# Performance work log

Hardware: AMD Instinct MI355X
Metric: run time of the kernel (lower is better)

Reference implementation:

```python
import jax, jax.numpy as jnp
import numpy as np

N_NODES = 100000
N_EDGES = 600000
D = 128
HEADS = 8
REL = 9
N_GRAPHS = 64


def _relconv(h, coeff, basis, w_loop, b, src, dst, etypes, n_nodes):
    # DGL RelGraphConv, basis regularizer (num_bases == num_rels), sum aggregation,
    # self-loop, bias, relu activation (dropout inactive at eval).
    W = jnp.einsum('rb,bio->rio', coeff, basis)  # [REL, D, D]
    hsrc = h[src]                                # [E, D] gather
    msg = jnp.zeros((hsrc.shape[0], W.shape[2]), h.dtype)
    for r in range(REL):  # small fixed relation set
        msg = msg + jnp.where((etypes == r)[:, None], hsrc @ W[r], 0.0)
    agg = jax.ops.segment_sum(msg, dst, num_segments=n_nodes)
    return jax.nn.relu(agg + h @ w_loop + b)


def _graph_norm(x, seg, n_graphs, w, b, ms):
    # scatter-based per-subgraph normalization (graphNorm)
    counts = jax.ops.segment_sum(jnp.ones((x.shape[0],), x.dtype), seg, num_segments=n_graphs)[:, None]
    mean = jax.ops.segment_sum(x, seg, num_segments=n_graphs) / counts
    sub = x - mean[seg] * ms
    var = jax.ops.segment_sum(sub * sub, seg, num_segments=n_graphs) / counts
    std = jnp.sqrt(var + 1e-6)
    return w * sub / std[seg] + b


def _layer_norm(x, g, b):
    mu = x.mean(-1, keepdims=True)
    v = jnp.mean((x - mu) ** 2, -1, keepdims=True)
    return g * (x - mu) / jnp.sqrt(v + 1e-5) + b


def _forward(h, src, dst, etypes, seg, num_graphs,
             q_coeff, q_basis, q_loop, q_bias,
             k_coeff, k_basis, k_loop, k_bias,
             v_coeff, v_basis, v_loop, v_bias,
             o_w, o_b, gn1_w, gn1_b, gn1_ms, ln1_g, ln1_b,
             gn2_w, gn2_b, gn2_ms, ffn1_w, ffn1_b, ffn2_w, ffn2_b,
             ln2_g, ln2_b):
    n = h.shape[0]
    hn = _graph_norm(h, seg, num_graphs, gn1_w, gn1_b, gn1_ms)
    Q = _relconv(hn, q_coeff, q_basis, q_loop, q_bias, src, dst, etypes, n)
    K = _relconv(hn, k_coeff, k_basis, k_loop, k_bias, src, dst, etypes, n)
    V = _relconv(hn, v_coeff, v_basis, v_loop, v_bias, src, dst, etypes, n)
    dh = D // HEADS
    Qh = Q.reshape(n, HEADS, dh)
    Kh = K.reshape(n, HEADS, dh)
    Vh = V.reshape(n, HEADS, dh)
    # edge dot-product attention: score_e = <K[src], Q[dst]> per head
    score = (Kh[src] * Qh[dst]).sum(-1, keepdims=True)            # [E, H, 1]
    score = jnp.exp(jnp.clip(score / np.float32(np.sqrt(dh)), -10.0, 10.0))
    wV = jax.ops.segment_sum(Vh[src] * score, dst, num_segments=n)  # [N, H, dh]
    z = jax.ops.segment_sum(score, dst, num_segments=n)             # [N, H, 1]
    attn = (wV / (z + 1e-6)).reshape(n, D)
    hO = attn @ o_w + o_b
    h1 = _layer_norm(hO, ln1_g, ln1_b)
    h2 = _graph_norm(h1, seg, num_graphs, gn2_w, gn2_b, gn2_ms)
    h3 = jax.nn.relu(h2 @ ffn1_w + ffn1_b) @ ffn2_w + ffn2_b
    return _layer_norm(h3, ln2_g, ln2_b)


def setup_inputs() -> dict:
    key = jax.random.key(0)
    ks = jax.random.split(key, 32)
    s = np.float32(1.0 / np.sqrt(D))
    inp = {
        'h': jax.random.normal(ks[0], (N_NODES, D), jnp.float32),
        'src': jax.random.randint(ks[1], (N_EDGES,), 0, N_NODES),
        'dst': jax.random.randint(ks[2], (N_EDGES,), 0, N_NODES),
        'etypes': jax.random.randint(ks[3], (N_EDGES,), 0, REL),
        'seg': jnp.sort(jax.random.randint(ks[4], (N_NODES,), 0, N_GRAPHS)),
        'num_graphs': N_GRAPHS,
    }
    def lin(k, i, o):
        return jax.random.normal(k, (i, o), jnp.float32) / np.float32(np.sqrt(i))
    for idx, nm in enumerate(['q', 'k', 'v']):
        base = 5 + idx * 4
        inp[nm + '_coeff'] = jax.random.normal(ks[base], (REL, REL), jnp.float32) / np.float32(np.sqrt(REL))
        inp[nm + '_basis'] = jax.random.normal(ks[base + 1], (REL, D, D), jnp.float32) * s
        inp[nm + '_loop'] = lin(ks[base + 2], D, D)
        inp[nm + '_bias'] = jnp.zeros((D,), jnp.float32)
    inp['o_w'] = lin(ks[17], D, D)
    inp['o_b'] = jnp.zeros((D,), jnp.float32)
    for nm in ['gn1', 'gn2']:
        inp[nm + '_w'] = jnp.ones((D,), jnp.float32)
        inp[nm + '_b'] = jnp.zeros((D,), jnp.float32)
        inp[nm + '_ms'] = jnp.ones((D,), jnp.float32)
    inp['ln1_g'] = jnp.ones((D,), jnp.float32)
    inp['ln1_b'] = jnp.zeros((D,), jnp.float32)
    inp['ln2_g'] = jnp.ones((D,), jnp.float32)
    inp['ln2_b'] = jnp.zeros((D,), jnp.float32)
    inp['ffn1_w'] = lin(ks[18], D, 2 * D)
    inp['ffn1_b'] = jnp.zeros((2 * D,), jnp.float32)
    inp['ffn2_w'] = lin(ks[19], 2 * D, D)
    inp['ffn2_b'] = jnp.zeros((D,), jnp.float32)
    return inp


def reference(h, src, dst, etypes, seg, num_graphs,
              q_coeff, q_basis, q_loop, q_bias,
              k_coeff, k_basis, k_loop, k_bias,
              v_coeff, v_basis, v_loop, v_bias,
              o_w, o_b, gn1_w, gn1_b, gn1_ms, ln1_g, ln1_b,
              gn2_w, gn2_b, gn2_ms, ffn1_w, ffn1_b, ffn2_w, ffn2_b,
              ln2_g, ln2_b):
    return _forward(h, src, dst, etypes, seg, num_graphs,
                    q_coeff, q_basis, q_loop, q_bias,
                    k_coeff, k_basis, k_loop, k_bias,
                    v_coeff, v_basis, v_loop, v_bias,
                    o_w, o_b, gn1_w, gn1_b, gn1_ms, ln1_g, ln1_b,
                    gn2_w, gn2_b, gn2_ms, ffn1_w, ffn1_b, ffn2_w, ffn2_b,
                    ln2_g, ln2_b)
```

## Files before the change

kernel.cpp:

```cpp
#include <hip/hip_runtime.h>
#include <math.h>

#define N_NODES 100000
#define N_EDGES 600000
#define D 128
#define REL 9
#define NG 64

typedef float f32x4 __attribute__((ext_vector_type(4)));
typedef _Float16 f16x8 __attribute__((ext_vector_type(8)));
typedef _Float16 h16x2 __attribute__((ext_vector_type(2)));

__device__ __forceinline__ ushort f2h(float x) {
    union { _Float16 h; ushort u; } c; c.h = (_Float16)x; return c.u;
}
__device__ __forceinline__ float h2f(ushort u) {
    union { ushort u; _Float16 h; } c; c.u = u; return (float)c.h;
}

__device__ __forceinline__ void ld16(const ushort* g, ushort* l) {
    __builtin_amdgcn_global_load_lds(
        (const __attribute__((address_space(1))) unsigned int*)g,
        (__attribute__((address_space(3))) unsigned int*)l, 16, 0, 0);
}

__device__ __forceinline__ int lbound(const int* __restrict__ a, int n, int key) {
    int lo = 0, hi = n;
    while (lo < hi) { int mid = (lo + hi) >> 1; if (a[mid] < key) lo = mid + 1; else hi = mid; }
    return lo;
}

__global__ void hist_kernel(const int* __restrict__ dst, int* __restrict__ cnt) {
    int e = blockIdx.x * 256 + threadIdx.x;
    if (e < N_EDGES) atomicAdd(&cnt[dst[e]], 1);
}

__global__ void scan1_kernel(const int* __restrict__ cnt, int* __restrict__ excl,
                             int* __restrict__ bsum, int n) {
    __shared__ int s[1024];
    int tid = threadIdx.x;
    int i = blockIdx.x * 1024 + tid;
    int v = (i < n) ? cnt[i] : 0;
    s[tid] = v;
    __syncthreads();
    for (int off = 1; off < 1024; off <<= 1) {
        int t = (tid >= off) ? s[tid - off] : 0;
        __syncthreads();
        s[tid] += t;
        __syncthreads();
    }
    if (i < n) excl[i] = s[tid] - v;
    if (tid == 1023) bsum[blockIdx.x] = s[1023];
}

__global__ void scan2_kernel(int* __restrict__ bsum, int nb) {
    __shared__ int s[128];
    int tid = threadIdx.x;
    int v = (tid < nb) ? bsum[tid] : 0;
    s[tid] = v;
    __syncthreads();
    for (int off = 1; off < 128; off <<= 1) {
        int t = (tid >= off) ? s[tid - off] : 0;
        __syncthreads();
        s[tid] += t;
        __syncthreads();
    }
    if (tid < nb) bsum[tid] = s[tid] - v;
}

__global__ void scan3_kernel(int* __restrict__ excl, const int* __restrict__ bsum, int n) {
    int i = blockIdx.x * 1024 + threadIdx.x;
    if (i < n) excl[i] += bsum[blockIdx.x];
}

__global__ void scatter_kernel(const int* __restrict__ src, const int* __restrict__ dst,
                               const int* __restrict__ ety, const int* __restrict__ estart,
                               int* __restrict__ cur, int* __restrict__ ssrc,
                               int* __restrict__ setp) {
    int e = blockIdx.x * 256 + threadIdx.x;
    if (e < N_EDGES) {
        int d = dst[e];
        int pos = estart[d] + atomicAdd(&cur[d], 1);
        ssrc[pos] = src[e];
        setp[pos] = ety[e];
    }
}

__global__ __launch_bounds__(256)
void gn_stats(const float* __restrict__ x, const int* __restrict__ seg,
              float* __restrict__ gsum, float* __restrict__ gsumsq) {
    int ch = threadIdx.x & 127;
    int rr = threadIdx.x >> 7;
    int n0 = blockIdx.x * 128;
    int nend = min(n0 + 128, N_NODES);
    float sx = 0.f, sxx = 0.f;
    int cg = -1;
    for (int n = n0 + rr; n < nend; n += 2) {
        int g = seg[n];
        if (g != cg) {
            if (cg >= 0) { atomicAdd(&gsum[cg * D + ch], sx); atomicAdd(&gsumsq[cg * D + ch], sxx); }
            cg = g; sx = 0.f; sxx = 0.f;
        }
        float v = x[(size_t)n * D + ch];
        sx += v; sxx += v * v;
    }
    if (cg >= 0) { atomicAdd(&gsum[cg * D + ch], sx); atomicAdd(&gsumsq[cg * D + ch], sxx); }
}

__global__ __launch_bounds__(256)
void gn_stats_h(const ushort* __restrict__ x, const int* __restrict__ seg,
                float* __restrict__ gsum, float* __restrict__ gsumsq) {
    int ch = threadIdx.x & 127;
    int rr = threadIdx.x >> 7;
    int n0 = blockIdx.x * 128;
    int nend = min(n0 + 128, N_NODES);
    float sx = 0.f, sxx = 0.f;
    int cg = -1;
    for (int n = n0 + rr; n < nend; n += 2) {
        int g = seg[n];
        if (g != cg) {
            if (cg >= 0) { atomicAdd(&gsum[cg * D + ch], sx); atomicAdd(&gsumsq[cg * D + ch], sxx); }
            cg = g; sx = 0.f; sxx = 0.f;
        }
        float v = h2f(x[(size_t)n * D + ch]);
        sx += v; sxx += v * v;
    }
    if (cg >= 0) { atomicAdd(&gsum[cg * D + ch], sx); atomicAdd(&gsumsq[cg * D + ch], sxx); }
}

__global__ void gn_final(const float* __restrict__ gsum, const float* __restrict__ gsumsq,
                         const int* __restrict__ seg, const float* __restrict__ w,
                         const float* __restrict__ b, const float* __restrict__ ms,
                         float* __restrict__ sc, float* __restrict__ off) {
    int g = blockIdx.x, ch = threadIdx.x;
    int lo = lbound(seg, N_NODES, g), hi = lbound(seg, N_NODES, g + 1);
    float cnt = (float)max(hi - lo, 1);
    float mean = gsum[g * D + ch] / cnt;
    float mm = mean * ms[ch];
    float var = gsumsq[g * D + ch] / cnt - 2.f * mm * mean + mm * mm;
    float rstd = rsqrtf(var + 1e-6f);
    float s = w[ch] * rstd;
    sc[g * D + ch] = s;
    off[g * D + ch] = b[ch] - s * mm;
}

__global__ __launch_bounds__(256)
void gn_apply(const float* __restrict__ x, const int* __restrict__ seg,
              const float* __restrict__ sc, const float* __restrict__ off,
              ushort* __restrict__ outhf) {
    int t = blockIdx.x * 256 + threadIdx.x;
    int n = t >> 6;
    if (n >= N_NODES) return;
    int ch = (t & 63) * 2;
    int g = seg[n];
    float2 xv = *(const float2*)&x[(size_t)n * D + ch];
    float2 s2 = *(const float2*)&sc[g * D + ch];
    float2 o2 = *(const float2*)&off[g * D + ch];
    ushort2 o;
    o.x = f2h(s2.x * xv.x + o2.x);
    o.y = f2h(s2.y * xv.y + o2.y);
    *(ushort2*)&outhf[(size_t)n * D + ch] = o;
}

__global__ __launch_bounds__(256)
void gn_apply_h(const ushort* __restrict__ x, const int* __restrict__ seg,
                const float* __restrict__ sc, const float* __restrict__ off,
                ushort* __restrict__ outhf) {
    int t = blockIdx.x * 256 + threadIdx.x;
    int n = t >> 6;
    if (n >= N_NODES) return;
    int ch = (t & 63) * 2;
    int g = seg[n];
    ushort2 xv = *(const ushort2*)&x[(size_t)n * D + ch];
    float2 s2 = *(const float2*)&sc[g * D + ch];
    float2 o2 = *(const float2*)&off[g * D + ch];
    ushort2 o;
    o.x = f2h(s2.x * h2f(xv.x) + o2.x);
    o.y = f2h(s2.y * h2f(xv.y) + o2.y);
    *(ushort2*)&outhf[(size_t)n * D + ch] = o;
}

__global__ void build_bt_qkv3(const float* __restrict__ c0, const float* __restrict__ c1,
                              const float* __restrict__ c2, const float* __restrict__ b0,
                              const float* __restrict__ b1, const float* __restrict__ b2,
                              const float* __restrict__ l0, const float* __restrict__ l1,
                              const float* __restrict__ l2, const float* __restrict__ i0,
                              const float* __restrict__ i1, const float* __restrict__ i2,
                              ushort* __restrict__ Btqkv, float* __restrict__ biasq) {
    int pj = blockIdx.y;
    const float* coeff  = pj == 0 ? c0 : (pj == 1 ? c1 : c2);
    const float* basis  = pj == 0 ? b0 : (pj == 1 ? b1 : b2);
    const float* loop_w = pj == 0 ? l0 : (pj == 1 ? l1 : l2);
    const float* bin    = pj == 0 ? i0 : (pj == 1 ? i1 : i2);
    ushort* Bt = Btqkv + (size_t)pj * 128 * 1280;
    int t = blockIdx.x * 256 + threadIdx.x;
    if (t < 128) biasq[pj * 128 + t] = bin[t];
    if (t >= 128 * 1280) return;
    int o = t / 1280;
    int k = t - o * 1280;
    float v;
    if (k < 128) {
        v = loop_w[k * 128 + o];
    } else {
        int kk = k - 128;
        int r = kk >> 7, i = kk & 127;
        v = 0.f;
#pragma unroll
        for (int b = 0; b < REL; ++b)
            v += coeff[r * REL + b] * basis[((size_t)b * 128 + i) * 128 + o];
    }
    Bt[(size_t)o * 1280 + k] = f2h(v);
}

__global__ void transpose_cast3(const float* __restrict__ o_w, ushort* __restrict__ Bto,
                                const float* __restrict__ f1, ushort* __restrict__ Btf1,
                                const float* __restrict__ f2, ushort* __restrict__ Btf2) {
    int t = blockIdx.x * 256 + threadIdx.x;
    if (t < 16384) {
        int n = t >> 7, k = t & 127;
        Bto[(size_t)n * 128 + k] = f2h(o_w[(size_t)k * 128 + n]);
    } else if (t < 49152) {
        int u = t - 16384;
        int n = u >> 7, k = u & 127;
        Btf1[(size_t)n * 128 + k] = f2h(f1[(size_t)k * 256 + n]);
    } else if (t < 81920) {
        int u = t - 49152;
        int n = u >> 8, k = u & 255;
        Btf2[(size_t)n * 256 + k] = f2h(f2[(size_t)k * 128 + n]);
    }
}

__global__ __launch_bounds__(256)
void s_pass(const ushort* __restrict__ hnhf, const int* __restrict__ ssrc,
            const int* __restrict__ setp, const int* __restrict__ estart,
            const int* __restrict__ ecnt, ushort* __restrict__ Ab, int c0, int c1) {
    int n = c0 + ((blockIdx.x * 256 + threadIdx.x) >> 6);
    if (n >= c1) return;
    int lane = threadIdx.x & 63;
    int e0 = estart[n], e1 = e0 + ecnt[n];
    h16x2 a0 = (h16x2)0, a1 = (h16x2)0, a2 = (h16x2)0, a3 = (h16x2)0, a4 = (h16x2)0;
    h16x2 a5 = (h16x2)0, a6 = (h16x2)0, a7 = (h16x2)0, a8 = (h16x2)0;
#define ACC(rr, hv) switch (rr) { \
        case 0: a0 += hv; break; case 1: a1 += hv; break; case 2: a2 += hv; break; \
        case 3: a3 += hv; break; case 4: a4 += hv; break; case 5: a5 += hv; break; \
        case 6: a6 += hv; break; case 7: a7 += hv; break; default: a8 += hv; break; }
    int e = e0;
    for (; e + 2 <= e1; e += 2) {
        int s0 = ssrc[e], s1 = ssrc[e + 1];
        int r0 = __builtin_amdgcn_readfirstlane(setp[e]);
        int r1 = __builtin_amdgcn_readfirstlane(setp[e + 1]);
        h16x2 hv0 = *(const h16x2*)&hnhf[(size_t)s0 * D + 2 * lane];
        h16x2 hv1 = *(const h16x2*)&hnhf[(size_t)s1 * D + 2 * lane];
        ACC(r0, hv0)
        ACC(r1, hv1)
    }
    if (e < e1) {
        int s0 = ssrc[e];
        int r0 = __builtin_amdgcn_readfirstlane(setp[e]);
        h16x2 hv0 = *(const h16x2*)&hnhf[(size_t)s0 * D + 2 * lane];
        ACC(r0, hv0)
    }
#undef ACC
    ushort* arow = Ab + (size_t)(n - c0) * 1152;
#define ST(r) *(h16x2*)&arow[r * 128 + 2 * lane] = a##r;
    ST(0) ST(1) ST(2) ST(3) ST(4) ST(5) ST(6) ST(7) ST(8)
#undef ST
}

template<bool SPLITA, bool RELU, bool F16OUT>
__global__ __launch_bounds__(256, 3)
void mfma_gemm(const ushort* __restrict__ A1, const ushort* __restrict__ A2, int lda2, int M,
               const ushort* __restrict__ Bt, int K,
               const float* __restrict__ bias, void* __restrict__ Cout, int ldc) {
    __shared__ ushort As[128 * 64];
    __shared__ ushort Bs[128 * 64];
    const int tid = threadIdx.x;
    const int lane = tid & 63;
    const int wave = tid >> 6;
    const int wm = wave & 1, wn = wave >> 1;
    const int quad = lane >> 4, l16 = lane & 15;
    const int col0 = blockIdx.x * 128, row0 = blockIdx.y * 128;

    const ushort* sA1[4];
    const ushort* sA2[4];
    const ushort* sB[4];
#pragma unroll
    for (int i = 0; i < 4; ++i) {
        int rs = (wave * 4 + i) * 8 + (lane >> 3);
        int kg = (lane & 7) ^ (rs & 7);
        int ra = row0 + rs; if (ra >= M) ra = M - 1;
        sA1[i] = SPLITA ? (A1 + (size_t)ra * 128 + kg * 8) : nullptr;
        sA2[i] = A2 + (size_t)ra * lda2 + kg * 8;
        sB[i]  = Bt + (size_t)(col0 + rs) * K + kg * 8;
    }

    f32x4 acc[4][4];
#pragma unroll
    for (int i = 0; i < 4; ++i)
#pragma unroll
        for (int j = 0; j < 4; ++j) acc[i][j] = (f32x4){0.f, 0.f, 0.f, 0.f};

    for (int kc = 0; kc < K; kc += 64) {
#pragma unroll
        for (int i = 0; i < 4; ++i) {
            const ushort* as = (SPLITA && kc < 128) ? (sA1[i] + kc) : (sA2[i] + (SPLITA ? kc - 128 : kc));
            ld16(as, &As[(wave * 4 + i) * 512]);
            ld16(sB[i] + kc, &Bs[(wave * 4 + i) * 512]);
        }
        __syncthreads();
#pragma unroll
        for (int h = 0; h < 2; ++h) {
            f16x8 af[4], bf[4];
#pragma unroll
            for (int i = 0; i < 4; ++i) {
                int r = wm * 64 + i * 16 + l16;
                af[i] = *(const f16x8*)&As[r * 64 + (((h * 4 + quad) ^ (r & 7)) * 8)];
                int c = wn * 64 + i * 16 + l16;
                bf[i] = *(const f16x8*)&Bs[c * 64 + (((h * 4 + quad) ^ (c & 7)) * 8)];
            }
#pragma unroll
            for (int i = 0; i < 4; ++i)
#pragma unroll
                for (int j = 0; j < 4; ++j)
                    acc[i][j] = __builtin_amdgcn_mfma_f32_16x16x32_f16(af[i], bf[j], acc[i][j], 0, 0, 0);
        }
        __syncthreads();
    }

#pragma unroll
    for (int i = 0; i < 4; ++i) {
        int gr0 = row0 + wm * 64 + i * 16 + quad * 4;
#pragma unroll
        for (int r = 0; r < 4; ++r) {
            int grow = gr0 + r;
            if (grow >= M) continue;
#pragma unroll
            for (int j = 0; j < 4; ++j) {
                int gcol = col0 + wn * 64 + j * 16 + l16;
                float v = acc[i][j][r] + bias[gcol];
                if (RELU) v = fmaxf(v, 0.f);
                if (F16OUT) ((ushort*)Cout)[(size_t)grow * ldc + gcol] = f2h(v);
                else        ((float*)Cout)[(size_t)grow * ldc + gcol] = v;
            }
        }
    }
}

template<bool F16OUT>
__global__ __launch_bounds__(256, 3)
void mfma_gemm_ln(const ushort* __restrict__ A, int lda, int M,
                  const ushort* __restrict__ Bt, int K,
                  const float* __restrict__ bias, const float* __restrict__ lng,
                  const float* __restrict__ lnb, void* __restrict__ Cout) {
    __shared__ ushort As[128 * 64];
    __shared__ ushort Bs[128 * 64];
    __shared__ float rsum[2][128];
    __shared__ float rsq[2][128];
    const int tid = threadIdx.x;
    const int lane = tid & 63;
    const int wave = tid >> 6;
    const int wm = wave & 1, wn = wave >> 1;
    const int quad = lane >> 4, l16 = lane & 15;
    const int row0 = blockIdx.y * 128;

    const ushort* sA[4];
    const ushort* sB[4];
#pragma unroll
    for (int i = 0; i < 4; ++i) {
        int rs = (wave * 4 + i) * 8 + (lane >> 3);
        int kg = (lane & 7) ^ (rs & 7);
        int ra = row0 + rs; if (ra >= M) ra = M - 1;
        sA[i] = A + (size_t)ra * lda + kg * 8;
        sB[i] = Bt + (size_t)rs * K + kg * 8;
    }

    f32x4 acc[4][4];
#pragma unroll
    for (int i = 0; i < 4; ++i)
#pragma unroll
        for (int j = 0; j < 4; ++j) acc[i][j] = (f32x4){0.f, 0.f, 0.f, 0.f};

    for (int kc = 0; kc < K; kc += 64) {
#pragma unroll
        for (int i = 0; i < 4; ++i) {
            ld16(sA[i] + kc, &As[(wave * 4 + i) * 512]);
            ld16(sB[i] + kc, &Bs[(wave * 4 + i) * 512]);
        }
        __syncthreads();
#pragma unroll
        for (int h = 0; h < 2; ++h) {
            f16x8 af[4], bf[4];
#pragma unroll
            for (int i = 0; i < 4; ++i) {
                int r = wm * 64 + i * 16 + l16;
                af[i] = *(const f16x8*)&As[r * 64 + (((h * 4 + quad) ^ (r & 7)) * 8)];
                int c = wn * 64 + i * 16 + l16;
                bf[i] = *(const f16x8*)&Bs[c * 64 + (((h * 4 + quad) ^ (c & 7)) * 8)];
            }
#pragma unroll
            for (int i = 0; i < 4; ++i)
#pragma unroll
                for (int j = 0; j < 4; ++j)
                    acc[i][j] = __builtin_amdgcn_mfma_f32_16x16x32_f16(af[i], bf[j], acc[i][j], 0, 0, 0);
        }
        __syncthreads();
    }

#pragma unroll
    for (int i = 0; i < 4; ++i) {
#pragma unroll
        for (int r = 0; r < 4; ++r) {
            float s = 0.f, q = 0.f;
#pragma unroll
            for (int j = 0; j < 4; ++j) {
                float v = acc[i][j][r] + bias[wn * 64 + j * 16 + l16];
                s += v; q += v * v;
            }
            s += __shfl_xor(s, 1); q += __shfl_xor(q, 1);
            s += __shfl_xor(s, 2); q += __shfl_xor(q, 2);
            s += __shfl_xor(s, 4); q += __shfl_xor(q, 4);
            s += __shfl_xor(s, 8); q += __shfl_xor(q, 8);
            if (l16 == 0) {
                int row = wm * 64 + i * 16 + quad * 4 + r;
                rsum[wn][row] = s;
                rsq[wn][row] = q;
            }
        }
    }
    __syncthreads();

#pragma unroll
    for (int i = 0; i < 4; ++i) {
#pragma unroll
        for (int r = 0; r < 4; ++r) {
            int row = wm * 64 + i * 16 + quad * 4 + r;
            int grow = row0 + row;
            if (grow >= M) continue;
            float tot = rsum[0][row] + rsum[1][row];
            float tq  = rsq[0][row] + rsq[1][row];
            float mu = tot * (1.f / 128.f);
            float var = tq * (1.f / 128.f) - mu * mu;
            float rstd = rsqrtf(var + 1e-5f);
#pragma unroll
            for (int j = 0; j < 4; ++j) {
                int gcol = wn * 64 + j * 16 + l16;
                float v = acc[i][j][r] + bias[gcol];
                float o = lng[gcol] * (v - mu) * rstd + lnb[gcol];
                if (F16OUT) ((ushort*)Cout)[(size_t)grow * 128 + gcol] = f2h(o);
                else        ((float*)Cout)[(size_t)grow * 128 + gcol] = o;
            }
        }
    }
}

__global__ __launch_bounds__(256)
void attn_kernel(const ushort* __restrict__ C, const int* __restrict__ ssrc,
                 const int* __restrict__ estart, const int* __restrict__ ecnt,
                 ushort* __restrict__ attnhf) {
    int n = (blockIdx.x * 256 + threadIdx.x) >> 6;
    if (n >= N_NODES) return;
    int lane = threadIdx.x & 63;
    h16x2 qh = *(const h16x2*)&C[(size_t)n * 384 + 2 * lane];
    int e0 = estart[n], e1 = e0 + ecnt[n];
    float wvx = 0.f, wvy = 0.f, z = 0.f;
    int e = e0;
    for (; e + 2 <= e1; e += 2) {
        int s0 = ssrc[e], s1 = ssrc[e + 1];
        h16x2 k0 = *(const h16x2*)&C[(size_t)s0 * 384 + 128 + 2 * lane];
        h16x2 k1 = *(const h16x2*)&C[(size_t)s1 * 384 + 128 + 2 * lane];
        h16x2 v0 = *(const h16x2*)&C[(size_t)s0 * 384 + 256 + 2 * lane];
        h16x2 v1 = *(const h16x2*)&C[(size_t)s1 * 384 + 256 + 2 * lane];
        float d0 = __builtin_amdgcn_fdot2(k0, qh, 0.f, false);
        float d1 = __builtin_amdgcn_fdot2(k1, qh, 0.f, false);
        d0 += __shfl_xor(d0, 1); d1 += __shfl_xor(d1, 1);
        d0 += __shfl_xor(d0, 2); d1 += __shfl_xor(d1, 2);
        d0 += __shfl_xor(d0, 4); d1 += __shfl_xor(d1, 4);
        float sc0 = __expf(fminf(fmaxf(d0 * 0.25f, -10.f), 10.f));
        float sc1 = __expf(fminf(fmaxf(d1 * 0.25f, -10.f), 10.f));
        wvx += sc0 * (float)v0.x + sc1 * (float)v1.x;
        wvy += sc0 * (float)v0.y + sc1 * (float)v1.y;
        z += sc0 + sc1;
    }
    if (e < e1) {
        int s0 = ssrc[e];
        h16x2 k0 = *(const h16x2*)&C[(size_t)s0 * 384 + 128 + 2 * lane];
        h16x2 v0 = *(const h16x2*)&C[(size_t)s0 * 384 + 256 + 2 * lane];
        float d0 = __builtin_amdgcn_fdot2(k0, qh, 0.f, false);
        d0 += __shfl_xor(d0, 1);
        d0 += __shfl_xor(d0, 2);
        d0 += __shfl_xor(d0, 4);
        float sc0 = __expf(fminf(fmaxf(d0 * 0.25f, -10.f), 10.f));
        wvx += sc0 * (float)v0.x;
        wvy += sc0 * (float)v0.y;
        z += sc0;
    }
    float inv = 1.f / (z + 1e-6f);
    ushort2 o;
    o.x = f2h(wvx * inv);
    o.y = f2h(wvy * inv);
    *(ushort2*)&attnhf[(size_t)n * D + 2 * lane] = o;
}

extern "C" void kernel_launch(void* const* d_in, const int* in_sizes, int n_in,
                              void* d_out, int out_size, void* d_ws, size_t ws_size,
                              hipStream_t stream) {
    (void)in_sizes; (void)n_in; (void)out_size;
    const float* h     = (const float*)d_in[0];
    const int*   src   = (const int*)d_in[1];
    const int*   dst   = (const int*)d_in[2];
    const int*   ety   = (const int*)d_in[3];
    const int*   seg   = (const int*)d_in[4];
    const float* coeffs[3] = {(const float*)d_in[6],  (const float*)d_in[10], (const float*)d_in[14]};
    const float* bases [3] = {(const float*)d_in[7],  (const float*)d_in[11], (const float*)d_in[15]};
    const float* loops [3] = {(const float*)d_in[8],  (const float*)d_in[12], (const float*)d_in[16]};
    const float* pbias [3] = {(const float*)d_in[9],  (const float*)d_in[13], (const float*)d_in[17]};
    const float* o_w   = (const float*)d_in[18];
    const float* o_b   = (const float*)d_in[19];
    const float* gn1_w = (const float*)d_in[20];
    const float* gn1_b = (const float*)d_in[21];
    const float* gn1_ms= (const float*)d_in[22];
    const float* gn2_w = (const float*)d_in[23];
    const float* gn2_b = (const float*)d_in[24];
    const float* gn2_ms= (const float*)d_in[25];
    const float* ln1_g = (const float*)d_in[26];
    const float* ln1_b = (const float*)d_in[27];
    const float* ln2_g = (const float*)d_in[28];
    const float* ln2_b = (const float*)d_in[29];
    const float* ffn1_w= (const float*)d_in[30];
    const float* ffn1_b= (const float*)d_in[31];
    const float* ffn2_w= (const float*)d_in[32];
    const float* ffn2_b= (const float*)d_in[33];

    char* p = (char*)d_ws;
    auto take = [&](size_t bytes) { char* r = p; p += (bytes + 255) & ~(size_t)255; return r; };
    int*    ecnt   = (int*)take((size_t)N_NODES * 4);
    int*    ecur   = (int*)take((size_t)N_NODES * 4);
    int*    estart = (int*)take((size_t)N_NODES * 4);
    int*    bsum   = (int*)take(512);
    int*    ssrc   = (int*)take((size_t)N_EDGES * 4);
    int*    setp   = (int*)take((size_t)N_EDGES * 4);
    float*  gsum   = (float*)take((size_t)NG * D * 4 * 2);
    float*  gsumsq = gsum + NG * D;
    float*  gsc    = (float*)take((size_t)NG * D * 4);
    float*  goff   = (float*)take((size_t)NG * D * 4);
    ushort* Btqkv  = (ushort*)take((size_t)384 * 1280 * 2);
    float*  biasq  = (float*)take(384 * 4);
    ushort* Bto    = (ushort*)take((size_t)128 * 128 * 2);
    ushort* Btf1   = (ushort*)take((size_t)256 * 128 * 2);
    ushort* Btf2   = (ushort*)take((size_t)128 * 256 * 2);
    ushort* hnhf   = (ushort*)take((size_t)N_NODES * D * 2);
    ushort* attnhf = (ushort*)take((size_t)N_NODES * D * 2);
    ushort* h1hf   = (ushort*)take((size_t)N_NODES * D * 2);
    ushort* Cqkv   = (ushort*)take((size_t)N_NODES * 384 * 2);
    size_t used = (size_t)(p - (char*)d_ws);
    size_t avail = (ws_size > used) ? ws_size - used : 0;
    int NC = 1;
    if (avail < (size_t)N_NODES * 1152 * 2) NC = 4;
    if (NC == 4 && avail < ((size_t)(N_NODES / 4 + 1) * 1152 * 2)) NC = 8;
    ushort* Ab = (ushort*)p;
    const int chunk = (N_NODES + NC - 1) / NC;

    ushort* gn2hf  = Cqkv;
    ushort* ffn1hf = (ushort*)((char*)Cqkv + 25600000);

    const int EB = (N_EDGES + 255) / 256;
    const int SB = (N_NODES + 1023) / 1024;
    const int WB = (N_NODES * 64 + 255) / 256;
    const int GB = (N_NODES + 127) / 128;
    const int RB = (N_NODES + 127) / 128;

    hipMemsetAsync(ecnt, 0, (size_t)((char*)(estart) - (char*)ecnt), stream);
    hist_kernel<<<EB, 256, 0, stream>>>(dst, ecnt);
    scan1_kernel<<<SB, 1024, 0, stream>>>(ecnt, estart, bsum, N_NODES);
    scan2_kernel<<<1, 128, 0, stream>>>(bsum, SB);
    scan3_kernel<<<SB, 1024, 0, stream>>>(estart, bsum, N_NODES);
    scatter_kernel<<<EB, 256, 0, stream>>>(src, dst, ety, estart, ecur, ssrc, setp);

    build_bt_qkv3<<<dim3(640, 3), 256, 0, stream>>>(
        coeffs[0], coeffs[1], coeffs[2], bases[0], bases[1], bases[2],
        loops[0], loops[1], loops[2], pbias[0], pbias[1], pbias[2], Btqkv, biasq);
    transpose_cast3<<<320, 256, 0, stream>>>(o_w, Bto, ffn1_w, Btf1, ffn2_w, Btf2);

    hipMemsetAsync(gsum, 0, (size_t)NG * D * 8, stream);
    gn_stats<<<GB, 256, 0, stream>>>(h, seg, gsum, gsumsq);
    gn_final<<<NG, 128, 0, stream>>>(gsum, gsumsq, seg, gn1_w, gn1_b, gn1_ms, gsc, goff);
    gn_apply<<<WB, 256, 0, stream>>>(h, seg, gsc, goff, hnhf);

    for (int c = 0; c < NC; ++c) {
        int c0 = c * chunk;
        int c1 = min(N_NODES, c0 + chunk);
        int rows = c1 - c0;
        if (rows <= 0) break;
        s_pass<<<(rows + 3) / 4, 256, 0, stream>>>(hnhf, ssrc, setp, estart, ecnt, Ab, c0, c1);
        mfma_gemm<true, true, true><<<dim3(3, (rows + 127) / 128), 256, 0, stream>>>(
            hnhf + (size_t)c0 * 128, Ab, 1152, rows, Btqkv, 1280, biasq,
            Cqkv + (size_t)c0 * 384, 384);
    }

    attn_kernel<<<WB, 256, 0, stream>>>(Cqkv, ssrc, estart, ecnt, attnhf);

    mfma_gemm_ln<true><<<dim3(1, RB), 256, 0, stream>>>(
        attnhf, 128, N_NODES, Bto, 128, o_b, ln1_g, ln1_b, h1hf);

    hipMemsetAsync(gsum, 0, (size_t)NG * D * 8, stream);
    gn_stats_h<<<GB, 256, 0, stream>>>(h1hf, seg, gsum, gsumsq);
    gn_final<<<NG, 128, 0, stream>>>(gsum, gsumsq, seg, gn2_w, gn2_b, gn2_ms, gsc, goff);
    gn_apply_h<<<WB, 256, 0, stream>>>(h1hf, seg, gsc, goff, gn2hf);

    mfma_gemm<false, true, true><<<dim3(2, RB), 256, 0, stream>>>(
        nullptr, gn2hf, 128, N_NODES, Btf1, 128, ffn1_b, ffn1hf, 256);
    mfma_gemm_ln<false><<<dim3(1, RB), 256, 0, stream>>>(
        ffn1hf, 256, N_NODES, Btf2, 256, ffn2_b, ln2_g, ln2_b, (float*)d_out);
}
```

Before: 769.8 us.

## Fuse per-relation neighbor aggregation into the QKV GEMM via relation-sorted CSR

Edges are now bucketed by (destination, relation) with a 9x-larger histogram and scan, so each node's edges of each relation are contiguous. The separate s_pass kernel that wrote a 1152-wide aggregated A matrix to global memory is removed. Instead a new 512-thread QKV GEMM gathers and sums neighbor features for each relation K-chunk directly into shared memory and covers all 384 output columns in one block. This drops the large intermediate write and read, but puts irregular gathers inside the GEMM's K loop without pipelining, and the gathers are repeated for both 64-wide halves of each relation.

```diff
diff --git a/kernel.cpp b/kernel.cpp
--- a/kernel.cpp
+++ b/kernel.cpp
@@ -6,6 +6,7 @@
 #define D 128
 #define REL 9
 #define NG 64
+#define NK9 (N_NODES * REL)
 
 typedef float f32x4 __attribute__((ext_vector_type(4)));
 typedef _Float16 f16x8 __attribute__((ext_vector_type(8)));
@@ -30,18 +31,21 @@
     return lo;
 }
 
-__global__ void hist_kernel(const int* __restrict__ dst, int* __restrict__ cnt) {
+__global__ void hist9_kernel(const int* __restrict__ dst, const int* __restrict__ ety,
+                             int* __restrict__ cnt9) {
     int e = blockIdx.x * 256 + threadIdx.x;
-    if (e < N_EDGES) atomicAdd(&cnt[dst[e]], 1);
-}
-
-__global__ void scan1_kernel(const int* __restrict__ cnt, int* __restrict__ excl,
-                             int* __restrict__ bsum, int n) {
+    if (e < N_EDGES) atomicAdd(&cnt9[dst[e] * REL + ety[e]], 1);
+}
+
+__global__ void scan1_8(const int* __restrict__ cnt, int* __restrict__ excl,
+                        int* __restrict__ bsum, int n) {
     __shared__ int s[1024];
     int tid = threadIdx.x;
-    int i = blockIdx.x * 1024 + tid;
-    int v = (i < n) ? cnt[i] : 0;
-    s[tid] = v;
+    int base = blockIdx.x * 8192 + tid * 8;
+    int v[8]; int sum = 0;
+#pragma unroll
+    for (int j = 0; j < 8; ++j) { v[j] = (base + j < n) ? cnt[base + j] : 0; sum += v[j]; }
+    s[tid] = sum;
     __syncthreads();
     for (int off = 1; off < 1024; off <<= 1) {
         int t = (tid >= off) ? s[tid - off] : 0;
@@ -49,7 +53,9 @@
         s[tid] += t;
         __syncthreads();
     }
-    if (i < n) excl[i] = s[tid] - v;
+    int run = s[tid] - sum;
+#pragma unroll
+    for (int j = 0; j < 8; ++j) { if (base + j < n) excl[base + j] = run; run += v[j]; }
     if (tid == 1023) bsum[blockIdx.x] = s[1023];
 }
 
@@ -68,21 +74,22 @@
     if (tid < nb) bsum[tid] = s[tid] - v;
 }
 
-__global__ void scan3_kernel(int* __restrict__ excl, const int* __restrict__ bsum, int n) {
-    int i = blockIdx.x * 1024 + threadIdx.x;
-    if (i < n) excl[i] += bsum[blockIdx.x];
-}
-
-__global__ void scatter_kernel(const int* __restrict__ src, const int* __restrict__ dst,
-                               const int* __restrict__ ety, const int* __restrict__ estart,
-                               int* __restrict__ cur, int* __restrict__ ssrc,
-                               int* __restrict__ setp) {
+__global__ void scan3_8(int* __restrict__ excl, const int* __restrict__ bsum, int n, int total) {
+    int base = blockIdx.x * 8192 + threadIdx.x * 8;
+    int add = bsum[blockIdx.x];
+#pragma unroll
+    for (int j = 0; j < 8; ++j) if (base + j < n) excl[base + j] += add;
+    if (blockIdx.x == 0 && threadIdx.x == 0) excl[n] = total;
+}
+
+__global__ void scatter9_kernel(const int* __restrict__ src, const int* __restrict__ dst,
+                                const int* __restrict__ ety, const int* __restrict__ rstart,
+                                int* __restrict__ cur9, int* __restrict__ ssrc) {
     int e = blockIdx.x * 256 + threadIdx.x;
     if (e < N_EDGES) {
-        int d = dst[e];
-        int pos = estart[d] + atomicAdd(&cur[d], 1);
+        int key = dst[e] * REL + ety[e];
+        int pos = rstart[key] + atomicAdd(&cur9[key], 1);
         ssrc[pos] = src[e];
-        setp[pos] = ety[e];
     }
 }
 
@@ -230,41 +237,111 @@
     }
 }
 
-__global__ __launch_bounds__(256)
-void s_pass(const ushort* __restrict__ hnhf, const int* __restrict__ ssrc,
-            const int* __restrict__ setp, const int* __restrict__ estart,
-            const int* __restrict__ ecnt, ushort* __restrict__ Ab, int c0, int c1) {
-    int n = c0 + ((blockIdx.x * 256 + threadIdx.x) >> 6);
-    if (n >= c1) return;
-    int lane = threadIdx.x & 63;
-    int e0 = estart[n], e1 = e0 + ecnt[n];
-    h16x2 a0 = (h16x2)0, a1 = (h16x2)0, a2 = (h16x2)0, a3 = (h16x2)0, a4 = (h16x2)0;
-    h16x2 a5 = (h16x2)0, a6 = (h16x2)0, a7 = (h16x2)0, a8 = (h16x2)0;
-#define ACC(rr, hv) switch (rr) { \
-        case 0: a0 += hv; break; case 1: a1 += hv; break; case 2: a2 += hv; break; \
-        case 3: a3 += hv; break; case 4: a4 += hv; break; case 5: a5 += hv; break; \
-        case 6: a6 += hv; break; case 7: a7 += hv; break; default: a8 += hv; break; }
-    int e = e0;
-    for (; e + 2 <= e1; e += 2) {
-        int s0 = ssrc[e], s1 = ssrc[e + 1];
-        int r0 = __builtin_amdgcn_readfirstlane(setp[e]);
-        int r1 = __builtin_amdgcn_readfirstlane(setp[e + 1]);
-        h16x2 hv0 = *(const h16x2*)&hnhf[(size_t)s0 * D + 2 * lane];
-        h16x2 hv1 = *(const h16x2*)&hnhf[(size_t)s1 * D + 2 * lane];
-        ACC(r0, hv0)
-        ACC(r1, hv1)
-    }
-    if (e < e1) {
-        int s0 = ssrc[e];
-        int r0 = __builtin_amdgcn_readfirstlane(setp[e]);
-        h16x2 hv0 = *(const h16x2*)&hnhf[(size_t)s0 * D + 2 * lane];
-        ACC(r0, hv0)
-    }
-#undef ACC
-    ushort* arow = Ab + (size_t)(n - c0) * 1152;
-#define ST(r) *(h16x2*)&arow[r * 128 + 2 * lane] = a##r;
-    ST(0) ST(1) ST(2) ST(3) ST(4) ST(5) ST(6) ST(7) ST(8)
-#undef ST
+__global__ __launch_bounds__(512, 2)
+void qkv_gemm_fused(const ushort* __restrict__ hnhf, const int* __restrict__ ssrc,
+                    const int* __restrict__ rstart, const ushort* __restrict__ Bt,
+                    const float* __restrict__ bias, ushort* __restrict__ Cout) {
+    __shared__ ushort As[128 * 64];
+    __shared__ ushort Bs[384 * 64];
+    const int tid = threadIdx.x;
+    const int lane = tid & 63;
+    const int wave = tid >> 6;
+    const int wm = wave & 1, wn = wave >> 1;
+    const int quad = lane >> 4, l16 = lane & 15;
+    const int row0 = blockIdx.x * 128;
+
+    const ushort* sA[2];
+#pragma unroll
+    for (int i = 0; i < 2; ++i) {
+        int rs = (wave * 2 + i) * 8 + (lane >> 3);
+        int kg = (lane & 7) ^ (rs & 7);
+        int ra = row0 + rs; if (ra >= N_NODES) ra = N_NODES - 1;
+        sA[i] = hnhf + (size_t)ra * D + kg * 8;
+    }
+    const ushort* sB[6];
+#pragma unroll
+    for (int i = 0; i < 6; ++i) {
+        int rs = (wave * 6 + i) * 8 + (lane >> 3);
+        int kg = (lane & 7) ^ (rs & 7);
+        sB[i] = Bt + (size_t)rs * 1280 + kg * 8;
+    }
+
+    const int grow = tid >> 2;
+    const int sub = tid & 3;
+    const int gnode = row0 + grow;
+    const int gvalid = (gnode < N_NODES);
+    const int gbase9 = gnode * REL;
+    const int rw = grow & 7;
+
+    f32x4 acc[4][6];
+#pragma unroll
+    for (int i = 0; i < 4; ++i)
+#pragma unroll
+        for (int j = 0; j < 6; ++j) acc[i][j] = (f32x4){0.f, 0.f, 0.f, 0.f};
+
+    for (int kc = 0; kc < 1280; kc += 64) {
+#pragma unroll
+        for (int i = 0; i < 6; ++i) ld16(sB[i] + kc, &Bs[(wave * 6 + i) * 512]);
+        if (kc < 128) {
+#pragma unroll
+            for (int i = 0; i < 2; ++i) ld16(sA[i] + kc, &As[(wave * 2 + i) * 512]);
+        } else {
+            int kk = kc - 128;
+            int r = kk >> 7;
+            int ch0 = kk & 64;
+            f16x8 a0 = (f16x8)0, a1 = (f16x8)0;
+            if (gvalid) {
+                int e0 = rstart[gbase9 + r];
+                int e1 = rstart[gbase9 + r + 1];
+                for (int e = e0; e < e1; ++e) {
+                    int s = ssrc[e];
+                    const f16x8* hp = (const f16x8*)&hnhf[(size_t)s * D + ch0 + sub * 16];
+                    a0 += hp[0];
+                    a1 += hp[1];
+                }
+            }
+            *(f16x8*)&As[grow * 64 + (((sub * 2) ^ rw) * 8)] = a0;
+            *(f16x8*)&As[grow * 64 + (((sub * 2 + 1) ^ rw) * 8)] = a1;
+        }
+        __syncthreads();
+#pragma unroll
+        for (int h = 0; h < 2; ++h) {
+            f16x8 af[4], bf[6];
+#pragma unroll
+            for (int i = 0; i < 4; ++i) {
+                int rr = wm * 64 + i * 16 + l16;
+                af[i] = *(const f16x8*)&As[rr * 64 + (((h * 4 + quad) ^ (rr & 7)) * 8)];
+            }
+#pragma unroll
+            for (int j = 0; j < 6; ++j) {
+                int cc = wn * 96 + j * 16 + l16;
+                bf[j] = *(const f16x8*)&Bs[cc * 64 + (((h * 4 + quad) ^ (cc & 7)) * 8)];
+            }
+#pragma unroll
+            for (int i = 0; i < 4; ++i)
+#pragma unroll
+                for (int j = 0; j < 6; ++j)
+                    acc[i][j] = __builtin_amdgcn_mfma_f32_16x16x32_f16(af[i], bf[j], acc[i][j], 0, 0, 0);
+        }
+        __syncthreads();
+    }
+
+#pragma unroll
+    for (int i = 0; i < 4; ++i) {
+        int gr0 = row0 + wm * 64 + i * 16 + quad * 4;
+#pragma unroll
+        for (int r = 0; r < 4; ++r) {
+            int gr = gr0 + r;
+            if (gr >= N_NODES) continue;
+#pragma unroll
+            for (int j = 0; j < 6; ++j) {
+                int gcol = wn * 96 + j * 16 + l16;
+                float v = acc[i][j][r] + bias[gcol];
+                v = fmaxf(v, 0.f);
+                Cout[(size_t)gr * 384 + gcol] = f2h(v);
+            }
+        }
+    }
 }
 
 template<bool SPLITA, bool RELU, bool F16OUT>
@@ -455,13 +532,12 @@
 
 __global__ __launch_bounds__(256)
 void attn_kernel(const ushort* __restrict__ C, const int* __restrict__ ssrc,
-                 const int* __restrict__ estart, const int* __restrict__ ecnt,
-                 ushort* __restrict__ attnhf) {
+                 const int* __restrict__ rstart, ushort* __restrict__ attnhf) {
     int n = (blockIdx.x * 256 + threadIdx.x) >> 6;
     if (n >= N_NODES) return;
     int lane = threadIdx.x & 63;
     h16x2 qh = *(const h16x2*)&C[(size_t)n * 384 + 2 * lane];
-    int e0 = estart[n], e1 = e0 + ecnt[n];
+    int e0 = rstart[n * REL], e1 = rstart[n * REL + REL];
     float wvx = 0.f, wvy = 0.f, z = 0.f;
     int e = e0;
     for (; e + 2 <= e1; e += 2) {
@@ -504,7 +580,7 @@
 extern "C" void kernel_launch(void* const* d_in, const int* in_sizes, int n_in,
                               void* d_out, int out_size, void* d_ws, size_t ws_size,
                               hipStream_t stream) {
-    (void)in_sizes; (void)n_in; (void)out_size;
+    (void)in_sizes; (void)n_in; (void)out_size; (void)ws_size;
     const float* h     = (const float*)d_in[0];
     const int*   src   = (const int*)d_in[1];
     const int*   dst   = (const int*)d_in[2];
@@ -533,12 +609,11 @@
 
     char* p = (char*)d_ws;
     auto take = [&](size_t bytes) { char* r = p; p += (bytes + 255) & ~(size_t)255; return r; };
-    int*    ecnt   = (int*)take((size_t)N_NODES * 4);
-    int*    ecur   = (int*)take((size_t)N_NODES * 4);
-    int*    estart = (int*)take((size_t)N_NODES * 4);
+    int*    cnt9   = (int*)take((size_t)NK9 * 2 * 4);
+    int*    cur9   = cnt9 + NK9;
+    int*    rstart = (int*)take((size_t)(NK9 + 8) * 4);
     int*    bsum   = (int*)take(512);
     int*    ssrc   = (int*)take((size_t)N_EDGES * 4);
-    int*    setp   = (int*)take((size_t)N_EDGES * 4);
     float*  gsum   = (float*)take((size_t)NG * D * 4 * 2);
     float*  gsumsq = gsum + NG * D;
     float*  gsc    = (float*)take((size_t)NG * D * 4);
@@ -552,29 +627,22 @@
     ushort* attnhf = (ushort*)take((size_t)N_NODES * D * 2);
     ushort* h1hf   = (ushort*)take((size_t)N_NODES * D * 2);
     ushort* Cqkv   = (ushort*)take((size_t)N_NODES * 384 * 2);
-    size_t used = (size_t)(p - (char*)d_ws);
-    size_t avail = (ws_size > used) ? ws_size - used : 0;
-    int NC = 1;
-    if (avail < (size_t)N_NODES * 1152 * 2) NC = 4;
-    if (NC == 4 && avail < ((size_t)(N_NODES / 4 + 1) * 1152 * 2)) NC = 8;
-    ushort* Ab = (ushort*)p;
-    const int chunk = (N_NODES + NC - 1) / NC;
 
     ushort* gn2hf  = Cqkv;
     ushort* ffn1hf = (ushort*)((char*)Cqkv + 25600000);
 
     const int EB = (N_EDGES + 255) / 256;
-    const int SB = (N_NODES + 1023) / 1024;
+    const int KB = (NK9 + 8191) / 8192;
     const int WB = (N_NODES * 64 + 255) / 256;
     const int GB = (N_NODES + 127) / 128;
     const int RB = (N_NODES + 127) / 128;
 
-    hipMemsetAsync(ecnt, 0, (size_t)((char*)(estart) - (char*)ecnt), stream);
-    hist_kernel<<<EB, 256, 0, stream>>>(dst, ecnt);
-    scan1_kernel<<<SB, 1024, 0, stream>>>(ecnt, estart, bsum, N_NODES);
-    scan2_kernel<<<1, 128, 0, stream>>>(bsum, SB);
-    scan3_kernel<<<SB, 1024, 0, stream>>>(estart, bsum, N_NODES);
-    scatter_kernel<<<EB, 256, 0, stream>>>(src, dst, ety, estart, ecur, ssrc, setp);
+    hipMemsetAsync(cnt9, 0, (size_t)NK9 * 8, stream);
+    hist9_kernel<<<EB, 256, 0, stream>>>(dst, ety, cnt9);
+    scan1_8<<<KB, 1024, 0, stream>>>(cnt9, rstart, bsum, NK9);
+    scan2_kernel<<<1, 128, 0, stream>>>(bsum, KB);
+    scan3_8<<<KB, 1024, 0, stream>>>(rstart, bsum, NK9, N_EDGES);
+    scatter9_kernel<<<EB, 256, 0, stream>>>(src, dst, ety, rstart, cur9, ssrc);
 
     build_bt_qkv3<<<dim3(640, 3), 256, 0, stream>>>(
         coeffs[0], coeffs[1], coeffs[2], bases[0], bases[1], bases[2],
@@ -586,18 +654,9 @@
     gn_final<<<NG, 128, 0, stream>>>(gsum, gsumsq, seg, gn1_w, gn1_b, gn1_ms, gsc, goff);
     gn_apply<<<WB, 256, 0, stream>>>(h, seg, gsc, goff, hnhf);
 
-    for (int c = 0; c < NC; ++c) {
-        int c0 = c * chunk;
-        int c1 = min(N_NODES, c0 + chunk);
-        int rows = c1 - c0;
-        if (rows <= 0) break;
-        s_pass<<<(rows + 3) / 4, 256, 0, stream>>>(hnhf, ssrc, setp, estart, ecnt, Ab, c0, c1);
-        mfma_gemm<true, true, true><<<dim3(3, (rows + 127) / 128), 256, 0, stream>>>(
-            hnhf + (size_t)c0 * 128, Ab, 1152, rows, Btqkv, 1280, biasq,
-            Cqkv + (size_t)c0 * 384, 384);
-    }
-
-    attn_kernel<<<WB, 256, 0, stream>>>(Cqkv, ssrc, estart, ecnt, attnhf);
+    qkv_gemm_fused<<<RB, 512, 0, stream>>>(hnhf, ssrc, rstart, Btqkv, biasq, Cqkv);
+
+    attn_kernel<<<WB, 256, 0, stream>>>(Cqkv, ssrc, rstart, attnhf);
 
     mfma_gemm_ln<true><<<dim3(1, RB), 256, 0, stream>>>(
         attnhf, 128, N_NODES, Bto, 128, o_b, ln1_g, ln1_b, h1hf);
```

New measurement: 790.5 us. 2.7% more time.
